# Kernel tuning notes

Measured on AMD Instinct MI355X. Metric: run time of the kernel, lower is better.

## Reference

```python
import jax, jax.numpy as jnp
import numpy as np

B, DIM1, DIM2, DIM3 = 4, 2048, 4096, 4096


def setup_inputs() -> dict:
    key = jax.random.key(0)
    k1, k2, k3 = jax.random.split(key, 3)
    x = jax.random.normal(k1, (B, DIM1, DIM2), dtype=jnp.float32)
    y = jax.random.normal(k2, (B, DIM1, DIM3), dtype=jnp.float32)
    weight = jax.random.normal(k3, (DIM2, DIM3), dtype=jnp.float32)
    return {"x": x, "y": y, "weight": weight}


def reference(x, y, weight):
    # Out = hardswish(mish(leaky_relu(x @ W, 0.01) + y)) + 0.5
    v = jnp.einsum('bik,kn->bin', x, weight)              # (B, dim1, dim3)
    v = jnp.where(v >= 0, v, 0.01 * v)                    # LeakyReLU(0.01)
    v = v + y
    v = v * jnp.tanh(jax.nn.softplus(v))                  # Mish
    relu6 = jnp.clip(v + 3.0, 0.0, 6.0)
    v = v * relu6 * (1.0 / 6.0) + 0.5                     # HardSwish + 0.5 (baked into kernel)
    return v
```

## Files before the change

### kernel.cpp

```cpp
#include <hip/hip_runtime.h>
#include <hip/hip_bf16.h>
#include <cstdint>

typedef __attribute__((ext_vector_type(8))) short short8;
typedef __attribute__((ext_vector_type(4))) float f32x4;
typedef unsigned short ushort_t;

#define MM 8192
#define NN 4096
#define KK 4096

#define BM 128
#define BN 128
#define BK 64

#define MFMA_BF16 __builtin_amdgcn_mfma_f32_16x16x32_bf16

__device__ __forceinline__ ushort_t f2bf(float f) {
  uint32_t u = __builtin_bit_cast(uint32_t, f);
  u = (u + 0x7FFFu + ((u >> 16) & 1u)) >> 16;
  return (ushort_t)u;
}

__device__ __forceinline__ float epilogue(float v, float yv) {
  v = fmaxf(v, 0.01f * v);
  v += yv;
  const float vc = fminf(v, 15.f);
  const float t = __builtin_amdgcn_exp2f(vc * 1.44269504f);
  const float d = t * t + 2.f * t;
  const float mi = v * d * __builtin_amdgcn_rcpf(d + 2.f);
  const float r6 = fminf(fmaxf(mi + 3.f, 0.f), 6.f);
  return mi * r6 * (1.f / 6.f) + 0.5f;
}

__device__ __forceinline__ void gload_lds16(const void* g, void* l) {
  __builtin_amdgcn_global_load_lds(
      (const __attribute__((address_space(1))) unsigned int*)g,
      (__attribute__((address_space(3))) unsigned int*)l, 16, 0, 0);
}

#define CVT_BLOCKS ((MM * KK) / (256 * 8))
#define WT_BLOCKS ((NN / 32) * (KK / 32))

template <int DO_X>
__global__ void prep_kernel(const float* __restrict__ X, ushort_t* __restrict__ XB,
                            const float* __restrict__ W, ushort_t* __restrict__ WT) {
  __shared__ float t[32][33];
  const int bid = blockIdx.x;
  const int tid = threadIdx.x;
  if (DO_X && bid < CVT_BLOCKS) {
    const size_t i = ((size_t)bid * 256 + tid) * 8;
    f32x4 v0 = __builtin_nontemporal_load(reinterpret_cast<const f32x4*>(&X[i]));
    f32x4 v1 = __builtin_nontemporal_load(reinterpret_cast<const f32x4*>(&X[i + 4]));
    short8 o;
    o[0] = (short)f2bf(v0[0]); o[1] = (short)f2bf(v0[1]);
    o[2] = (short)f2bf(v0[2]); o[3] = (short)f2bf(v0[3]);
    o[4] = (short)f2bf(v1[0]); o[5] = (short)f2bf(v1[1]);
    o[6] = (short)f2bf(v1[2]); o[7] = (short)f2bf(v1[3]);
    *reinterpret_cast<short8*>(&XB[i]) = o;
  } else {
    const int b2 = DO_X ? (bid - CVT_BLOCKS) : bid;
    const int n0 = (b2 & 127) * 32, k0 = (b2 >> 7) * 32;
    const int tx = tid & 31, ty = tid >> 5;
#pragma unroll
    for (int i = ty; i < 32; i += 8)
      t[i][tx] = __builtin_nontemporal_load(&W[(size_t)(k0 + i) * NN + n0 + tx]);
    __syncthreads();
#pragma unroll
    for (int i = ty; i < 32; i += 8)
      WT[(size_t)(n0 + i) * KK + k0 + tx] = f2bf(t[tx][i]);
  }
}

__global__ __launch_bounds__(256, 4) void gemm_bf16(
    const ushort_t* __restrict__ XB, const ushort_t* __restrict__ WT,
    const float* __restrict__ Y, float* __restrict__ O) {
  __shared__ ushort_t As[BM * BK];
  __shared__ ushort_t Bs[BN * BK];

  const int wg = blockIdx.x;
  const int xcd = wg & 7;
  const int local = wg >> 3;
  const int bm0 = (local >> 2) * BM;
  const int bn0 = (xcd * 4 + (local & 3)) * BN;

  const int tid = threadIdx.x;
  const int lane = tid & 63;
  const int wid = tid >> 6;
  const int wm = (wid >> 1) * 64, wn = (wid & 1) * 64;
  const int lr = lane & 15, lg = lane >> 4, lr7 = lane & 7;

  const int s_sub = lane >> 3;
  const int s_chunk = (lane & 7) ^ s_sub;
  const int srow = wid * 32 + s_sub;
  const ushort_t* aB = XB + (size_t)(bm0 + srow) * KK + s_chunk * 8;
  const ushort_t* bB = WT + (size_t)(bn0 + srow) * KK + s_chunk * 8;
  ushort_t* aL = As + wid * 4 * 512;
  ushort_t* bL = Bs + wid * 4 * 512;

  const int aRow = (wm + lr) * BK;
  const int bRow = (wn + lr) * BK;
  const int slot0 = ((lg ^ lr7) << 3);
  const int slot1 = (((4 | lg) ^ lr7) << 3);
  const ushort_t* a0 = As + aRow + slot0;
  const ushort_t* a1 = As + aRow + slot1;
  const ushort_t* b0 = Bs + bRow + slot0;
  const ushort_t* b1 = Bs + bRow + slot1;

  f32x4 acc[4][4] = {};

  for (int kt = 0; kt < KK; kt += BK) {
    __syncthreads();
#pragma unroll
    for (int j = 0; j < 4; ++j)
      gload_lds16(aB + (size_t)j * 8 * KK + kt, aL + j * 512);
#pragma unroll
    for (int j = 0; j < 4; ++j)
      gload_lds16(bB + (size_t)j * 8 * KK + kt, bL + j * 512);
    __syncthreads();

#pragma unroll
    for (int ks = 0; ks < 2; ++ks) {
      const ushort_t* ap = ks ? a1 : a0;
      const ushort_t* bp = ks ? b1 : b0;
      short8 a[4], b[4];
#pragma unroll
      for (int i = 0; i < 4; ++i) {
        a[i] = *reinterpret_cast<const short8*>(ap + i * 16 * BK);
        b[i] = *reinterpret_cast<const short8*>(bp + i * 16 * BK);
      }
#pragma unroll
      for (int i = 0; i < 4; ++i)
#pragma unroll
        for (int j = 0; j < 4; ++j)
          acc[i][j] = MFMA_BF16(a[i], b[j], acc[i][j], 0, 0, 0);
    }
  }

#pragma unroll
  for (int i = 0; i < 4; ++i) {
#pragma unroll
    for (int j = 0; j < 4; ++j) {
#pragma unroll
      for (int r = 0; r < 4; ++r) {
        const int grow = bm0 + wm + i * 16 + lg * 4 + r;
        const int gcol = bn0 + wn + j * 16 + lr;
        const size_t idx = (size_t)grow * NN + gcol;
        const float yv = __builtin_nontemporal_load(&Y[idx]);
        __builtin_nontemporal_store(epilogue(acc[i][j][r], yv), &O[idx]);
      }
    }
  }
}

#define LDP 72
__global__ __launch_bounds__(256, 3) void gemm_fused(
    const float* __restrict__ X, const ushort_t* __restrict__ WT,
    const float* __restrict__ Y, float* __restrict__ O) {
  __shared__ ushort_t Asm[BM * LDP];
  __shared__ ushort_t Bsm[BN * LDP];

  const int nwg = (MM / BM) * (NN / BN);
  int wg = blockIdx.x;
  wg = (wg % 8) * (nwg / 8) + wg / 8;
  const int NT = NN / BN;
  const int bm0 = (wg / NT) * BM;
  const int bn0 = (wg % NT) * BN;

  const int tid = threadIdx.x;
  const int lane = tid & 63;
  const int wid = tid >> 6;
  const int wm = (wid >> 1) * 64, wn = (wid & 1) * 64;
  const int lr = lane & 15, lg = lane >> 4;

  f32x4 acc[4][4] = {};

  const int arow = tid >> 2;
  const int ac = (tid & 3) * 4;
  const int brow = tid >> 1;
  const int bc0 = (tid & 1) * 32;

  for (int kt = 0; kt < KK; kt += BK) {
    __syncthreads();
#pragma unroll
    for (int p = 0; p < 2; ++p) {
      const int row = arow + p * 64;
      const float* src = &X[(size_t)(bm0 + row) * KK + kt];
#pragma unroll
      for (int j = 0; j < 4; ++j) {
        f32x4 v = *reinterpret_cast<const f32x4*>(&src[ac + j * 16]);
        uint2 packed;
        packed.x = (uint32_t)f2bf(v[0]) | ((uint32_t)f2bf(v[1]) << 16);
        packed.y = (uint32_t)f2bf(v[2]) | ((uint32_t)f2bf(v[3]) << 16);
        *reinterpret_cast<uint2*>(&Asm[row * LDP + ac + j * 16]) = packed;
      }
    }
    {
      const ushort_t* src = &WT[(size_t)(bn0 + brow) * KK + kt + bc0];
#pragma unroll
      for (int j = 0; j < 4; ++j) {
        short8 u = *reinterpret_cast<const short8*>(&src[j * 8]);
        *reinterpret_cast<short8*>(&Bsm[brow * LDP + bc0 + j * 8]) = u;
      }
    }
    __syncthreads();

#pragma unroll
    for (int ks = 0; ks < 2; ++ks) {
      short8 a[4], b[4];
#pragma unroll
      for (int i = 0; i < 4; ++i) {
        a[i] = *reinterpret_cast<const short8*>(&Asm[(wm + i * 16 + lr) * LDP + ks * 32 + lg * 8]);
        b[i] = *reinterpret_cast<const short8*>(&Bsm[(wn + i * 16 + lr) * LDP + ks * 32 + lg * 8]);
      }
#pragma unroll
      for (int i = 0; i < 4; ++i)
#pragma unroll
        for (int j = 0; j < 4; ++j)
          acc[i][j] = MFMA_BF16(a[i], b[j], acc[i][j], 0, 0, 0);
    }
  }

#pragma unroll
  for (int i = 0; i < 4; ++i) {
#pragma unroll
    for (int j = 0; j < 4; ++j) {
#pragma unroll
      for (int r = 0; r < 4; ++r) {
        const int grow = bm0 + wm + i * 16 + lg * 4 + r;
        const int gcol = bn0 + wn + j * 16 + lr;
        const size_t idx = (size_t)grow * NN + gcol;
        O[idx] = epilogue(acc[i][j][r], Y[idx]);
      }
    }
  }
}

__global__ void naive_fused(const float* __restrict__ X, const float* __restrict__ W,
                            const float* __restrict__ Y, float* __restrict__ O) {
  const int n0 = (blockIdx.x * 256 + threadIdx.x) * 4;
  const int m = blockIdx.y;
  f32x4 acc = {0.f, 0.f, 0.f, 0.f};
  const float* xr = &X[(size_t)m * KK];
  for (int k = 0; k < KK; ++k) {
    const float xv = xr[k];
    const f32x4 wv = *reinterpret_cast<const f32x4*>(&W[(size_t)k * NN + n0]);
    acc[0] += xv * wv[0];
    acc[1] += xv * wv[1];
    acc[2] += xv * wv[2];
    acc[3] += xv * wv[3];
  }
  const size_t idx = (size_t)m * NN + n0;
  O[idx + 0] = epilogue(acc[0], Y[idx + 0]);
  O[idx + 1] = epilogue(acc[1], Y[idx + 1]);
  O[idx + 2] = epilogue(acc[2], Y[idx + 2]);
  O[idx + 3] = epilogue(acc[3], Y[idx + 3]);
}

extern "C" void kernel_launch(void* const* d_in, const int* in_sizes, int n_in,
                              void* d_out, int out_size, void* d_ws, size_t ws_size,
                              hipStream_t stream) {
  const float* x = (const float*)d_in[0];
  const float* y = (const float*)d_in[1];
  const float* w = (const float*)d_in[2];
  float* out = (float*)d_out;

  const size_t xb_bytes = (size_t)MM * KK * sizeof(ushort_t);
  const size_t wt_bytes = (size_t)NN * KK * sizeof(ushort_t);

  if (ws_size >= xb_bytes + wt_bytes) {
    ushort_t* XB = (ushort_t*)d_ws;
    ushort_t* WT = (ushort_t*)((char*)d_ws + xb_bytes);
    hipLaunchKernelGGL((prep_kernel<1>), dim3(CVT_BLOCKS + WT_BLOCKS), dim3(256), 0, stream,
                       x, XB, w, WT);
    hipLaunchKernelGGL(gemm_bf16, dim3((MM / BM) * (NN / BN)), dim3(256), 0, stream,
                       XB, WT, y, out);
  } else if (ws_size >= wt_bytes) {
    ushort_t* WT = (ushort_t*)d_ws;
    hipLaunchKernelGGL((prep_kernel<0>), dim3(WT_BLOCKS), dim3(256), 0, stream,
                       x, nullptr, w, WT);
    hipLaunchKernelGGL(gemm_fused, dim3((MM / BM) * (NN / BN)), dim3(256), 0, stream,
                       x, WT, y, out);
  } else {
    hipLaunchKernelGGL(naive_fused, dim3(NN / 1024, MM), dim3(256), 0, stream, x, w, y, out);
  }
}
```

Baseline: 339.6 us.

## Replace 128x128 bf16 GEMM with 256x256 double-buffered 8-wave pipelined kernel

The bf16 GEMM path moves from 128x128 tiles with 4 waves and a single LDS buffer to 256x256 tiles with 8 waves, each computing 128x64. LDS is double-buffered, and global-to-LDS staging for the next tiles is interleaved with four MFMA quadrants per K-step. Those phases are separated by explicit barriers, waitcnt fences and s_setprio. The larger tile raises arithmetic intensity, and the staged prefetch hides load latency that the old kernel exposed behind two syncthreads per iteration. In exchange it uses 128KB of LDS per block and many more accumulator registers. The hand-tuned waitcnt counts are fragile, and the wrap-around prefetch indexing loads extra tiles past the end of K.

Measured after the change: 330.5 us. 2.7% less time.

```diff
diff --git a/kernel.cpp b/kernel.cpp
--- a/kernel.cpp
+++ b/kernel.cpp
@@ -13,6 +13,7 @@
 #define BM 128
 #define BN 128
 #define BK 64
+#define NT (KK / BK)
 
 #define MFMA_BF16 __builtin_amdgcn_mfma_f32_16x16x32_bf16
 
@@ -72,82 +73,153 @@
   }
 }
 
-__global__ __launch_bounds__(256, 4) void gemm_bf16(
+#define LDSE 32768
+
+#define STAGE_A(buf, h, kt)                                                    \
+  {                                                                            \
+    const int r_ = (h) * 64 + wid * 8;                                         \
+    gload_lds16(XB + (size_t)(bm0 + r_ + l8) * KK + (kt) + sslot * 8,          \
+                &lds[(buf) * LDSE + r_ * 64]);                                 \
+    gload_lds16(XB + (size_t)(bm0 + r_ + 128 + l8) * KK + (kt) + sslot * 8,    \
+                &lds[(buf) * LDSE + (r_ + 128) * 64]);                         \
+  }
+
+#define STAGE_B(buf, qn, kt)                                                   \
+  {                                                                            \
+    const int r_ = (qn) * 32 + (wid >> 2) * 64 + (wid & 3) * 8;                \
+    gload_lds16(WT + (size_t)(bn0 + r_ + l8) * KK + (kt) + sslot * 8,          \
+                &lds[(buf) * LDSE + 16384 + r_ * 64]);                         \
+    gload_lds16(WT + (size_t)(bn0 + r_ + 128 + l8) * KK + (kt) + sslot * 8,    \
+                &lds[(buf) * LDSE + 16384 + (r_ + 128) * 64]);                 \
+  }
+
+#define LOAD_A(dst, buf, qm)                                                   \
+  _Pragma("unroll") for (int i = 0; i < 4; ++i) {                              \
+    dst[0][i] = *reinterpret_cast<const short8*>(                              \
+        &lds[(buf) * LDSE + aOff + (qm) * 4096 + i * 1024 + slot0]);           \
+    dst[1][i] = *reinterpret_cast<const short8*>(                              \
+        &lds[(buf) * LDSE + aOff + (qm) * 4096 + i * 1024 + slot1]);           \
+  }
+
+#define LOAD_B(dst, buf, qn)                                                   \
+  _Pragma("unroll") for (int jj = 0; jj < 2; ++jj) {                           \
+    dst[0][jj] = *reinterpret_cast<const short8*>(                             \
+        &lds[(buf) * LDSE + bOff + (qn) * 2048 + jj * 1024 + slot0]);          \
+    dst[1][jj] = *reinterpret_cast<const short8*>(                             \
+        &lds[(buf) * LDSE + bOff + (qn) * 2048 + jj * 1024 + slot1]);          \
+  }
+
+#define MFMA_QUAD(AF, BF, QM, QN)                                              \
+  __builtin_amdgcn_s_setprio(1);                                               \
+  _Pragma("unroll") for (int ks = 0; ks < 2; ++ks)                             \
+      _Pragma("unroll") for (int i = 0; i < 4; ++i)                            \
+          _Pragma("unroll") for (int jj = 0; jj < 2; ++jj)                     \
+              acc[(QM) * 4 + i][(QN) * 2 + jj] =                               \
+      MFMA_BF16(AF[ks][i], BF[ks][jj], acc[(QM) * 4 + i][(QN) * 2 + jj], 0, 0, 0); \
+  __builtin_amdgcn_s_setprio(0);
+
+#define BAR()                          \
+  __builtin_amdgcn_sched_barrier(0);   \
+  __builtin_amdgcn_s_barrier();        \
+  __builtin_amdgcn_sched_barrier(0)
+
+#define WAIT_LGKM0()                                   \
+  asm volatile("s_waitcnt lgkmcnt(0)" ::: "memory");   \
+  __builtin_amdgcn_sched_barrier(0)
+
+#define TILE_BODY(cur, nxt, t)                                                 \
+  {                                                                            \
+    const int k1 = (((t) + 1) & (NT - 1)) * BK;                                \
+    const int k2 = (((t) + 2) & (NT - 1)) * BK;                                \
+                                                  \
+    LOAD_A(a, cur, 0);                                                         \
+    LOAD_B(b0, cur, 0);                                                        \
+    STAGE_A(nxt, 1, k1);                                                       \
+    asm volatile("s_waitcnt lgkmcnt(8)" ::: "memory");                         \
+    BAR();                                                                     \
+    WAIT_LGKM0();                                                              \
+    MFMA_QUAD(a, b0, 0, 0);                                                    \
+    BAR();                                                                     \
+                                                  \
+    LOAD_B(b1, cur, 1);                                                        \
+    STAGE_A(cur, 0, k2);                                                       \
+    BAR();                                                                     \
+    WAIT_LGKM0();                                                              \
+    MFMA_QUAD(a, b1, 0, 1);                                                    \
+    BAR();                                                                     \
+                                                  \
+    LOAD_A(a, cur, 1);                                                         \
+    STAGE_B(cur, 0, k2);                                                       \
+    BAR();                                                                     \
+    WAIT_LGKM0();                                                              \
+    MFMA_QUAD(a, b1, 1, 1);                                                    \
+    BAR();                                                                     \
+                                                  \
+    STAGE_B(cur, 1, k2);                                                       \
+    asm volatile("s_waitcnt vmcnt(6)" ::: "memory");                           \
+    BAR();                                                                     \
+    MFMA_QUAD(a, b0, 1, 0);                                                    \
+    BAR();                                                                     \
+  }
+
+__global__ __launch_bounds__(512, 2) void gemm_bf16_256(
     const ushort_t* __restrict__ XB, const ushort_t* __restrict__ WT,
     const float* __restrict__ Y, float* __restrict__ O) {
-  __shared__ ushort_t As[BM * BK];
-  __shared__ ushort_t Bs[BN * BK];
+  __shared__ ushort_t lds[2 * LDSE];
 
   const int wg = blockIdx.x;
   const int xcd = wg & 7;
   const int local = wg >> 3;
-  const int bm0 = (local >> 2) * BM;
-  const int bn0 = (xcd * 4 + (local & 3)) * BN;
+  const int bm0 = (local >> 1) * 256;
+  const int bn0 = (xcd * 2 + (local & 1)) * 256;
 
   const int tid = threadIdx.x;
   const int lane = tid & 63;
   const int wid = tid >> 6;
-  const int wm = (wid >> 1) * 64, wn = (wid & 1) * 64;
+  const int wmi = wid >> 2;
+  const int wni = wid & 3;
+
+  const int l8 = lane >> 3;
+  const int sslot = (lane & 7) ^ l8;
+
   const int lr = lane & 15, lg = lane >> 4, lr7 = lane & 7;
-
-  const int s_sub = lane >> 3;
-  const int s_chunk = (lane & 7) ^ s_sub;
-  const int srow = wid * 32 + s_sub;
-  const ushort_t* aB = XB + (size_t)(bm0 + srow) * KK + s_chunk * 8;
-  const ushort_t* bB = WT + (size_t)(bn0 + srow) * KK + s_chunk * 8;
-  ushort_t* aL = As + wid * 4 * 512;
-  ushort_t* bL = Bs + wid * 4 * 512;
-
-  const int aRow = (wm + lr) * BK;
-  const int bRow = (wn + lr) * BK;
-  const int slot0 = ((lg ^ lr7) << 3);
-  const int slot1 = (((4 | lg) ^ lr7) << 3);
-  const ushort_t* a0 = As + aRow + slot0;
-  const ushort_t* a1 = As + aRow + slot1;
-  const ushort_t* b0 = Bs + bRow + slot0;
-  const ushort_t* b1 = Bs + bRow + slot1;
-
-  f32x4 acc[4][4] = {};
-
-  for (int kt = 0; kt < KK; kt += BK) {
-    __syncthreads();
-#pragma unroll
-    for (int j = 0; j < 4; ++j)
-      gload_lds16(aB + (size_t)j * 8 * KK + kt, aL + j * 512);
-#pragma unroll
-    for (int j = 0; j < 4; ++j)
-      gload_lds16(bB + (size_t)j * 8 * KK + kt, bL + j * 512);
-    __syncthreads();
-
-#pragma unroll
-    for (int ks = 0; ks < 2; ++ks) {
-      const ushort_t* ap = ks ? a1 : a0;
-      const ushort_t* bp = ks ? b1 : b0;
-      short8 a[4], b[4];
-#pragma unroll
-      for (int i = 0; i < 4; ++i) {
-        a[i] = *reinterpret_cast<const short8*>(ap + i * 16 * BK);
-        b[i] = *reinterpret_cast<const short8*>(bp + i * 16 * BK);
-      }
-#pragma unroll
-      for (int i = 0; i < 4; ++i)
-#pragma unroll
-        for (int j = 0; j < 4; ++j)
-          acc[i][j] = MFMA_BF16(a[i], b[j], acc[i][j], 0, 0, 0);
-    }
-  }
-
-#pragma unroll
-  for (int i = 0; i < 4; ++i) {
-#pragma unroll
-    for (int j = 0; j < 4; ++j) {
+  const int slot0 = (lg ^ lr7) * 8;
+  const int slot1 = ((4 | lg) ^ lr7) * 8;
+  const int aOff = (wmi * 128 + lr) * 64;
+  const int bOff = 16384 + (wni * 64 + lr) * 64;
+
+  f32x4 acc[8][4] = {};
+  short8 a[2][4], b0[2][2], b1[2][2];
+
+  STAGE_A(0, 0, 0);
+  STAGE_B(0, 0, 0);
+  STAGE_B(0, 1, 0);
+  STAGE_A(0, 1, 0);
+  asm volatile("s_waitcnt vmcnt(4)" ::: "memory");
+  STAGE_A(1, 0, BK);
+  STAGE_B(1, 0, BK);
+  STAGE_B(1, 1, BK);
+  asm volatile("s_waitcnt vmcnt(6)" ::: "memory");
+  BAR();
+
+#pragma unroll 1
+  for (int t = 0; t < NT; t += 2) {
+    TILE_BODY(0, 1, t);
+    TILE_BODY(1, 0, t + 1);
+  }
+  asm volatile("s_waitcnt vmcnt(0)" ::: "memory");
+
+#pragma unroll
+  for (int mi = 0; mi < 8; ++mi) {
+#pragma unroll
+    for (int nj = 0; nj < 4; ++nj) {
 #pragma unroll
       for (int r = 0; r < 4; ++r) {
-        const int grow = bm0 + wm + i * 16 + lg * 4 + r;
-        const int gcol = bn0 + wn + j * 16 + lr;
+        const int grow = bm0 + wmi * 128 + mi * 16 + lg * 4 + r;
+        const int gcol = bn0 + wni * 64 + nj * 16 + lr;
         const size_t idx = (size_t)grow * NN + gcol;
         const float yv = __builtin_nontemporal_load(&Y[idx]);
-        __builtin_nontemporal_store(epilogue(acc[i][j][r], yv), &O[idx]);
+        __builtin_nontemporal_store(epilogue(acc[mi][nj][r], yv), &O[idx]);
       }
     }
   }
@@ -163,9 +235,9 @@
   const int nwg = (MM / BM) * (NN / BN);
   int wg = blockIdx.x;
   wg = (wg % 8) * (nwg / 8) + wg / 8;
-  const int NT = NN / BN;
-  const int bm0 = (wg / NT) * BM;
-  const int bn0 = (wg % NT) * BN;
+  const int NTC = NN / BN;
+  const int bm0 = (wg / NTC) * BM;
+  const int bn0 = (wg % NTC) * BN;
 
   const int tid = threadIdx.x;
   const int lane = tid & 63;
@@ -273,7 +345,7 @@
     ushort_t* WT = (ushort_t*)((char*)d_ws + xb_bytes);
     hipLaunchKernelGGL((prep_kernel<1>), dim3(CVT_BLOCKS + WT_BLOCKS), dim3(256), 0, stream,
                        x, XB, w, WT);
-    hipLaunchKernelGGL(gemm_bf16, dim3((MM / BM) * (NN / BN)), dim3(256), 0, stream,
+    hipLaunchKernelGGL(gemm_bf16_256, dim3((MM / 256) * (NN / 256)), dim3(512), 0, stream,
                        XB, WT, y, out);
   } else if (ws_size >= wt_bytes) {
     ushort_t* WT = (ushort_t*)d_ws;
```

## Replace bf16 GEMM with 256x128 8-wave ping-pong pipelined kernel

Applied to the files above, without the earlier changes.

Replaces the simple load-sync-compute bf16 GEMM with a 512-thread, 256x128 tile kernel. Half-tiles of A and B are staged into LDS in phases interleaved with MFMA quadrants, using explicit waitcnt, barriers and setprio so global-to-LDS loads overlap compute. The aim is to hide memory latency and cut the idle time around the two __syncthreads per K-step. The hand-tuned waitcnt counts and barrier placement are fragile, and the kernel keeps a single LDS buffer that is reused within each iteration.

Result: slower. 508.4 us (+49.7%).

```diff
diff --git a/kernel.cpp b/kernel.cpp
--- a/kernel.cpp
+++ b/kernel.cpp
@@ -13,6 +13,7 @@
 #define BM 128
 #define BN 128
 #define BK 64
+#define NT (KK / BK)
 
 #define MFMA_BF16 __builtin_amdgcn_mfma_f32_16x16x32_bf16
 
@@ -72,69 +73,115 @@
   }
 }
 
-__global__ __launch_bounds__(256, 4) void gemm_bf16(
+#define STAGE_A(H, ktv)                                                        \
+  gload_lds16(XB + uA##H##0 + (ktv) + vstage, &As[rA(H, 0) * 64]);             \
+  gload_lds16(XB + uA##H##1 + (ktv) + vstage, &As[rA(H, 1) * 64]);
+
+#define STAGE_B(H, ktv)                                                        \
+  gload_lds16(WT + uB##H + (ktv) + vstage, &Bs[rB(H) * 64]);
+
+#define rA(H, Q) (((Q)*2 + (wid >> 2)) * 64 + (wid & 3) * 8 + (H)*32)
+#define rB(H) ((wid >> 2) * 64 + (wid & 3) * 8 + (H)*32)
+
+#define LOAD_A2(qm)                                                            \
+  _Pragma("unroll") for (int mi = 0; mi < 2; ++mi) {                           \
+    a[0][mi] = *reinterpret_cast<const short8*>(                               \
+        &As[aBase + (qm)*2048 + mi * 1024 + slot0]);                           \
+    a[1][mi] = *reinterpret_cast<const short8*>(                               \
+        &As[aBase + (qm)*2048 + mi * 1024 + slot1]);                           \
+  }
+
+#define LOAD_B2(dst, qn)                                                       \
+  _Pragma("unroll") for (int nj = 0; nj < 2; ++nj) {                           \
+    dst[0][nj] = *reinterpret_cast<const short8*>(                             \
+        &Bs[bBase + (qn)*2048 + nj * 1024 + slot0]);                           \
+    dst[1][nj] = *reinterpret_cast<const short8*>(                             \
+        &Bs[bBase + (qn)*2048 + nj * 1024 + slot1]);                           \
+  }
+
+#define MFMA_PHASE(QM, QN, BF)                                                 \
+  __builtin_amdgcn_s_setprio(1);                                               \
+  _Pragma("unroll") for (int ks = 0; ks < 2; ++ks)                             \
+      _Pragma("unroll") for (int mi = 0; mi < 2; ++mi)                         \
+          _Pragma("unroll") for (int nj = 0; nj < 2; ++nj)                     \
+              acc[(QM)*2 + mi][(QN)*2 + nj] =                                  \
+      MFMA_BF16(a[ks][mi], BF[ks][nj], acc[(QM)*2 + mi][(QN)*2 + nj], 0, 0, 0);\
+  __builtin_amdgcn_s_setprio(0);
+
+#define BAR() __builtin_amdgcn_s_barrier()
+
+__global__ __launch_bounds__(512, 4) void gemm_bf16_mp(
     const ushort_t* __restrict__ XB, const ushort_t* __restrict__ WT,
     const float* __restrict__ Y, float* __restrict__ O) {
-  __shared__ ushort_t As[BM * BK];
-  __shared__ ushort_t Bs[BN * BK];
+  __shared__ ushort_t As[256 * 64];
+  __shared__ ushort_t Bs[128 * 64];
 
   const int wg = blockIdx.x;
   const int xcd = wg & 7;
   const int local = wg >> 3;
-  const int bm0 = (local >> 2) * BM;
-  const int bn0 = (xcd * 4 + (local & 3)) * BN;
+  const int bm0 = (local >> 2) * 256;
+  const int bn0 = (xcd * 4 + (local & 3)) * 128;
 
   const int tid = threadIdx.x;
   const int lane = tid & 63;
   const int wid = tid >> 6;
-  const int wm = (wid >> 1) * 64, wn = (wid & 1) * 64;
+  const int wmi = wid >> 1;
+  const int wni = wid & 1;
+
+  const int l8 = lane >> 3;
+  const uint32_t vstage = (uint32_t)l8 * KK + ((lane & 7) ^ l8) * 8;
+  const uint32_t uA00 = (uint32_t)(bm0 + rA(0, 0)) * KK;
+  const uint32_t uA01 = (uint32_t)(bm0 + rA(0, 1)) * KK;
+  const uint32_t uA10 = (uint32_t)(bm0 + rA(1, 0)) * KK;
+  const uint32_t uA11 = (uint32_t)(bm0 + rA(1, 1)) * KK;
+  const uint32_t uB0 = (uint32_t)(bn0 + rB(0)) * KK;
+  const uint32_t uB1 = (uint32_t)(bn0 + rB(1)) * KK;
+
   const int lr = lane & 15, lg = lane >> 4, lr7 = lane & 7;
-
-  const int s_sub = lane >> 3;
-  const int s_chunk = (lane & 7) ^ s_sub;
-  const int srow = wid * 32 + s_sub;
-  const ushort_t* aB = XB + (size_t)(bm0 + srow) * KK + s_chunk * 8;
-  const ushort_t* bB = WT + (size_t)(bn0 + srow) * KK + s_chunk * 8;
-  ushort_t* aL = As + wid * 4 * 512;
-  ushort_t* bL = Bs + wid * 4 * 512;
-
-  const int aRow = (wm + lr) * BK;
-  const int bRow = (wn + lr) * BK;
-  const int slot0 = ((lg ^ lr7) << 3);
-  const int slot1 = (((4 | lg) ^ lr7) << 3);
-  const ushort_t* a0 = As + aRow + slot0;
-  const ushort_t* a1 = As + aRow + slot1;
-  const ushort_t* b0 = Bs + bRow + slot0;
-  const ushort_t* b1 = Bs + bRow + slot1;
+  const int slot0 = (lg ^ lr7) * 8;
+  const int slot1 = ((4 | lg) ^ lr7) * 8;
+  const int aBase = (wmi * 64 + lr) * 64;
+  const int bBase = (wni * 64 + lr) * 64;
 
   f32x4 acc[4][4] = {};
-
-  for (int kt = 0; kt < KK; kt += BK) {
-    __syncthreads();
-#pragma unroll
-    for (int j = 0; j < 4; ++j)
-      gload_lds16(aB + (size_t)j * 8 * KK + kt, aL + j * 512);
-#pragma unroll
-    for (int j = 0; j < 4; ++j)
-      gload_lds16(bB + (size_t)j * 8 * KK + kt, bL + j * 512);
-    __syncthreads();
-
-#pragma unroll
-    for (int ks = 0; ks < 2; ++ks) {
-      const ushort_t* ap = ks ? a1 : a0;
-      const ushort_t* bp = ks ? b1 : b0;
-      short8 a[4], b[4];
-#pragma unroll
-      for (int i = 0; i < 4; ++i) {
-        a[i] = *reinterpret_cast<const short8*>(ap + i * 16 * BK);
-        b[i] = *reinterpret_cast<const short8*>(bp + i * 16 * BK);
-      }
-#pragma unroll
-      for (int i = 0; i < 4; ++i)
-#pragma unroll
-        for (int j = 0; j < 4; ++j)
-          acc[i][j] = MFMA_BF16(a[i], b[j], acc[i][j], 0, 0, 0);
-    }
+  short8 a[2][2], b0[2][2], b1[2][2];
+
+  STAGE_B(0, 0);
+  STAGE_A(0, 0);
+  STAGE_B(1, 0);
+  asm volatile("s_waitcnt vmcnt(1)" ::: "memory");
+  BAR();
+
+#pragma unroll 1
+  for (int t = 0; t < NT; ++t) {
+    const int kt = t * BK;
+    const int k1 = ((t + 1) & (NT - 1)) * BK;
+    LOAD_A2(0);
+    LOAD_B2(b0, 0);
+    STAGE_A(1, kt);
+    asm volatile("s_waitcnt lgkmcnt(4)");
+    BAR();
+    asm volatile("s_waitcnt lgkmcnt(0)");
+    MFMA_PHASE(0, 0, b0);
+    asm volatile("s_waitcnt vmcnt(2)" ::: "memory");
+    BAR();
+    LOAD_B2(b1, 1);
+    STAGE_B(0, k1);
+    BAR();
+    asm volatile("s_waitcnt lgkmcnt(0)");
+    MFMA_PHASE(0, 1, b1);
+    asm volatile("s_waitcnt vmcnt(1)" ::: "memory");
+    BAR();
+    LOAD_A2(1);
+    STAGE_A(0, k1);
+    STAGE_B(1, k1);
+    asm volatile("s_waitcnt lgkmcnt(4)");
+    BAR();
+    asm volatile("s_waitcnt lgkmcnt(0)");
+    MFMA_PHASE(1, 1, b1);
+    MFMA_PHASE(1, 0, b0);
+    asm volatile("s_waitcnt vmcnt(1)" ::: "memory");
+    BAR();
   }
 
 #pragma unroll
@@ -143,8 +190,8 @@
     for (int j = 0; j < 4; ++j) {
 #pragma unroll
       for (int r = 0; r < 4; ++r) {
-        const int grow = bm0 + wm + i * 16 + lg * 4 + r;
-        const int gcol = bn0 + wn + j * 16 + lr;
+        const int grow = bm0 + wmi * 64 + i * 16 + lg * 4 + r;
+        const int gcol = bn0 + wni * 64 + j * 16 + lr;
         const size_t idx = (size_t)grow * NN + gcol;
         const float yv = __builtin_nontemporal_load(&Y[idx]);
         __builtin_nontemporal_store(epilogue(acc[i][j][r], yv), &O[idx]);
@@ -163,9 +210,9 @@
   const int nwg = (MM / BM) * (NN / BN);
   int wg = blockIdx.x;
   wg = (wg % 8) * (nwg / 8) + wg / 8;
-  const int NT = NN / BN;
-  const int bm0 = (wg / NT) * BM;
-  const int bn0 = (wg % NT) * BN;
+  const int NTC = NN / BN;
+  const int bm0 = (wg / NTC) * BM;
+  const int bn0 = (wg % NTC) * BN;
 
   const int tid = threadIdx.x;
   const int lane = tid & 63;
@@ -273,7 +320,7 @@
     ushort_t* WT = (ushort_t*)((char*)d_ws + xb_bytes);
     hipLaunchKernelGGL((prep_kernel<1>), dim3(CVT_BLOCKS + WT_BLOCKS), dim3(256), 0, stream,
                        x, XB, w, WT);
-    hipLaunchKernelGGL(gemm_bf16, dim3((MM / BM) * (NN / BN)), dim3(256), 0, stream,
+    hipLaunchKernelGGL(gemm_bf16_mp, dim3((MM / 256) * (NN / 128)), dim3(512), 0, stream,
                        XB, WT, y, out);
   } else if (ws_size >= wt_bytes) {
     ushort_t* WT = (ushort_t*)d_ws;
```

## Use 256x256 tiles, 32x32 MFMA, and double-buffered LDS in bf16 GEMM

Applied to the files above, without the earlier changes.

Replaces the 128x128 single-buffered GEMM with a 512-thread, 256x256 tile kernel that uses 32x32x16 bf16 MFMA. The next K-tile is loaded into a second LDS buffer while the current one is consumed, leaving one barrier per iteration. The goal is higher arithmetic intensity per LDS byte and overlap of global loads with MFMA work. The cost is 128KB of LDS and many accumulator registers, which limits occupancy, and the loop issues one redundant wrap-around prefetch on its last iteration.

Measured after the change: 332.1 us. 1.02x faster.

```diff
diff --git a/kernel.cpp b/kernel.cpp
--- a/kernel.cpp
+++ b/kernel.cpp
@@ -4,6 +4,7 @@
 
 typedef __attribute__((ext_vector_type(8))) short short8;
 typedef __attribute__((ext_vector_type(4))) float f32x4;
+typedef __attribute__((ext_vector_type(16))) float f32x16;
 typedef unsigned short ushort_t;
 
 #define MM 8192
@@ -13,8 +14,10 @@
 #define BM 128
 #define BN 128
 #define BK 64
+#define NT (KK / BK)
 
 #define MFMA_BF16 __builtin_amdgcn_mfma_f32_16x16x32_bf16
+#define MFMA32 __builtin_amdgcn_mfma_f32_32x32x16_bf16
 
 __device__ __forceinline__ ushort_t f2bf(float f) {
   uint32_t u = __builtin_bit_cast(uint32_t, f);
@@ -72,82 +75,88 @@
   }
 }
 
-__global__ __launch_bounds__(256, 4) void gemm_bf16(
+#define HB 32768
+
+#define STAGE(base, kt)                                                        \
+  _Pragma("unroll") for (int c = 0; c < 4; ++c) {                              \
+    gload_lds16(XB + offA[c] + (kt), (base) + (wid * 8 + c * 64) * 64);        \
+    gload_lds16(WT + offB[c] + (kt),                                           \
+                (base) + 16384 + (wid * 8 + c * 64) * 64);                     \
+  }
+
+__global__ __launch_bounds__(512, 2) void gemm_bf16_v5(
     const ushort_t* __restrict__ XB, const ushort_t* __restrict__ WT,
     const float* __restrict__ Y, float* __restrict__ O) {
-  __shared__ ushort_t As[BM * BK];
-  __shared__ ushort_t Bs[BN * BK];
+  __shared__ ushort_t sh[2 * HB];
 
   const int wg = blockIdx.x;
   const int xcd = wg & 7;
   const int local = wg >> 3;
-  const int bm0 = (local >> 2) * BM;
-  const int bn0 = (xcd * 4 + (local & 3)) * BN;
+  const int bm0 = (local >> 1) * 256;
+  const int bn0 = (xcd * 2 + (local & 1)) * 256;
 
   const int tid = threadIdx.x;
   const int lane = tid & 63;
   const int wid = tid >> 6;
-  const int wm = (wid >> 1) * 64, wn = (wid & 1) * 64;
-  const int lr = lane & 15, lg = lane >> 4, lr7 = lane & 7;
-
-  const int s_sub = lane >> 3;
-  const int s_chunk = (lane & 7) ^ s_sub;
-  const int srow = wid * 32 + s_sub;
-  const ushort_t* aB = XB + (size_t)(bm0 + srow) * KK + s_chunk * 8;
-  const ushort_t* bB = WT + (size_t)(bn0 + srow) * KK + s_chunk * 8;
-  ushort_t* aL = As + wid * 4 * 512;
-  ushort_t* bL = Bs + wid * 4 * 512;
-
-  const int aRow = (wm + lr) * BK;
-  const int bRow = (wn + lr) * BK;
-  const int slot0 = ((lg ^ lr7) << 3);
-  const int slot1 = (((4 | lg) ^ lr7) << 3);
-  const ushort_t* a0 = As + aRow + slot0;
-  const ushort_t* a1 = As + aRow + slot1;
-  const ushort_t* b0 = Bs + bRow + slot0;
-  const ushort_t* b1 = Bs + bRow + slot1;
-
-  f32x4 acc[4][4] = {};
-
-  for (int kt = 0; kt < KK; kt += BK) {
-    __syncthreads();
-#pragma unroll
-    for (int j = 0; j < 4; ++j)
-      gload_lds16(aB + (size_t)j * 8 * KK + kt, aL + j * 512);
-#pragma unroll
-    for (int j = 0; j < 4; ++j)
-      gload_lds16(bB + (size_t)j * 8 * KK + kt, bL + j * 512);
-    __syncthreads();
-
-#pragma unroll
-    for (int ks = 0; ks < 2; ++ks) {
-      const ushort_t* ap = ks ? a1 : a0;
-      const ushort_t* bp = ks ? b1 : b0;
-      short8 a[4], b[4];
-#pragma unroll
-      for (int i = 0; i < 4; ++i) {
-        a[i] = *reinterpret_cast<const short8*>(ap + i * 16 * BK);
-        b[i] = *reinterpret_cast<const short8*>(bp + i * 16 * BK);
-      }
-#pragma unroll
-      for (int i = 0; i < 4; ++i)
-#pragma unroll
-        for (int j = 0; j < 4; ++j)
-          acc[i][j] = MFMA_BF16(a[i], b[j], acc[i][j], 0, 0, 0);
-    }
-  }
-
-#pragma unroll
-  for (int i = 0; i < 4; ++i) {
-#pragma unroll
-    for (int j = 0; j < 4; ++j) {
-#pragma unroll
-      for (int r = 0; r < 4; ++r) {
-        const int grow = bm0 + wm + i * 16 + lg * 4 + r;
-        const int gcol = bn0 + wn + j * 16 + lr;
+  const int wmi = wid >> 2;
+  const int wni = wid & 3;
+
+  const int l8 = lane >> 3;
+  const uint32_t vsw = (uint32_t)l8 * KK + ((lane & 7) ^ l8) * 8;
+  uint32_t offA[4], offB[4];
+#pragma unroll
+  for (int c = 0; c < 4; ++c) {
+    offA[c] = (uint32_t)(bm0 + wid * 8 + c * 64) * KK + vsw;
+    offB[c] = (uint32_t)(bn0 + wid * 8 + c * 64) * KK + vsw;
+  }
+
+  const int l31 = lane & 31, kh = lane >> 5, l7 = lane & 7;
+  const int aBase = (wmi * 128 + l31) * 64;
+  const int bBase = 16384 + (wni * 64 + l31) * 64;
+  int sl[4];
+#pragma unroll
+  for (int ks = 0; ks < 4; ++ks) sl[ks] = ((ks * 2 + kh) ^ l7) * 8;
+
+  f32x16 acc[4][2] = {};
+
+  STAGE(sh, 0);
+  __syncthreads();
+
+#pragma unroll 1
+  for (int t = 0; t < NT; ++t) {
+    ushort_t* cur = sh + (t & 1) * HB;
+    ushort_t* nxt = sh + ((t + 1) & 1) * HB;
+    const int k1 = ((t + 1) & (NT - 1)) * BK;
+    STAGE(nxt, k1);
+#pragma unroll
+    for (int ks = 0; ks < 4; ++ks) {
+      short8 av[4], bv[2];
+#pragma unroll
+      for (int mf = 0; mf < 4; ++mf)
+        av[mf] = *reinterpret_cast<const short8*>(&cur[aBase + mf * 2048 + sl[ks]]);
+#pragma unroll
+      for (int nf = 0; nf < 2; ++nf)
+        bv[nf] = *reinterpret_cast<const short8*>(&cur[bBase + nf * 2048 + sl[ks]]);
+#pragma unroll
+      for (int mf = 0; mf < 4; ++mf)
+#pragma unroll
+        for (int nf = 0; nf < 2; ++nf)
+          acc[mf][nf] = MFMA32(av[mf], bv[nf], acc[mf][nf], 0, 0, 0);
+    }
+    __syncthreads();
+  }
+
+#pragma unroll
+  for (int mf = 0; mf < 4; ++mf) {
+#pragma unroll
+    for (int nf = 0; nf < 2; ++nf) {
+#pragma unroll
+      for (int r = 0; r < 16; ++r) {
+        const int grow = bm0 + wmi * 128 + mf * 32 + (r & 3) + 8 * (r >> 2) + 4 * kh;
+        const int gcol = bn0 + wni * 64 + nf * 32 + l31;
         const size_t idx = (size_t)grow * NN + gcol;
         const float yv = __builtin_nontemporal_load(&Y[idx]);
-        __builtin_nontemporal_store(epilogue(acc[i][j][r], yv), &O[idx]);
+        __builtin_nontemporal_store(epilogue(acc[mf][nf][r], yv), &O[idx]);
       }
     }
   }
@@ -163,9 +172,9 @@
   const int nwg = (MM / BM) * (NN / BN);
   int wg = blockIdx.x;
   wg = (wg % 8) * (nwg / 8) + wg / 8;
-  const int NT = NN / BN;
-  const int bm0 = (wg / NT) * BM;
-  const int bn0 = (wg % NT) * BN;
+  const int NTC = NN / BN;
+  const int bm0 = (wg / NTC) * BM;
+  const int bn0 = (wg % NTC) * BN;
 
   const int tid = threadIdx.x;
   const int lane = tid & 63;
@@ -273,7 +282,7 @@
     ushort_t* WT = (ushort_t*)((char*)d_ws + xb_bytes);
     hipLaunchKernelGGL((prep_kernel<1>), dim3(CVT_BLOCKS + WT_BLOCKS), dim3(256), 0, stream,
                        x, XB, w, WT);
-    hipLaunchKernelGGL(gemm_bf16, dim3((MM / BM) * (NN / BN)), dim3(256), 0, stream,
+    hipLaunchKernelGGL(gemm_bf16_v5, dim3((MM / 256) * (NN / 256)), dim3(512), 0, stream,
                        XB, WT, y, out);
   } else if (ws_size >= wt_bytes) {
     ushort_t* WT = (ushort_t*)d_ws;
```
